# Optimization experiments

Hardware: AMD Instinct MI355X
Metric: run time of the kernel (lower is better)

## Reference

```python
import jax, jax.numpy as jnp
import numpy as np

B, N, C = 8, 2048, 256
H = 8
D = C // H
HID = 4 * C
EPS = 1e-5


def _layernorm(x, g, b):
    m = jnp.mean(x, axis=-1, keepdims=True)
    v = jnp.mean((x - m) ** 2, axis=-1, keepdims=True)
    return (x - m) * jax.lax.rsqrt(v + EPS) * g + b


def setup_inputs() -> dict:
    key = jax.random.key(0)
    ks = jax.random.split(key, 8)
    s = 0.02
    return {
        "x": jax.random.normal(ks[0], (B, N, C), dtype=jnp.float32),
        "ln1_g": jnp.ones((C,), jnp.float32),
        "ln1_b": jnp.zeros((C,), jnp.float32),
        "qkv_w": jax.random.normal(ks[1], (3 * C, C), jnp.float32) * s,  # torch Linear: (out,in), no bias
        "scale": jnp.asarray(D ** -0.5, jnp.float32),  # learnable temperature scalar
        "proj_w": jax.random.normal(ks[2], (C, C), jnp.float32) * s,
        "proj_b": jnp.zeros((C,), jnp.float32),
        "ln2_g": jnp.ones((C,), jnp.float32),
        "ln2_b": jnp.zeros((C,), jnp.float32),
        "fc1_w": jax.random.normal(ks[3], (HID, C), jnp.float32) * s,
        "fc1_b": jnp.zeros((HID,), jnp.float32),
        "fc2_w": jax.random.normal(ks[4], (C, HID), jnp.float32) * s,
        "fc2_b": jnp.zeros((C,), jnp.float32),
    }


def _attn(x, qkv_w, scale, proj_w, proj_b):
    b, n, c = x.shape
    qkv = (x @ qkv_w.T).reshape(b, n, 3, H, D)
    qkv = jnp.transpose(qkv, (2, 0, 3, 1, 4))  # (3, B, H, N, D)
    q, k, v = qkv[0], qkv[1], qkv[2]
    attn = jnp.einsum("bhnd,bhmd->bhnm", q, k) * scale  # full NxN scores (faithful)
    eye = jnp.eye(n, dtype=bool)
    attn = jnp.where(eye, -jnp.inf, attn)  # mask diagonal (no self-relation)
    attn = jax.nn.softmax(attn, axis=-1)
    out = jnp.einsum("bhnm,bhmd->bhnd", attn, v)
    out = jnp.transpose(out, (0, 2, 1, 3)).reshape(b, n, c)
    return out @ proj_w.T + proj_b


def reference(x, ln1_g, ln1_b, qkv_w, scale, proj_w, proj_b,
              ln2_g, ln2_b, fc1_w, fc1_b, fc2_w, fc2_b):
    x = x + _attn(_layernorm(x, ln1_g, ln1_b), qkv_w, scale, proj_w, proj_b)
    h = _layernorm(x, ln2_g, ln2_b)
    h = jax.nn.gelu(h @ fc1_w.T + fc1_b, approximate=False)  # torch GELU default = exact
    x = x + (h @ fc2_w.T + fc2_b)
    return x
```

## Files before the change

### kernel.cpp

```cpp
#include <hip/hip_runtime.h>
#include <cstdint>
#include <cstddef>


typedef __bf16 bf16x8 __attribute__((ext_vector_type(8)));
typedef __bf16 bf16x4 __attribute__((ext_vector_type(4)));
typedef float  f32x4  __attribute__((ext_vector_type(4)));

#define BN_TOK   2048
#define CC       256
#define HID_DIM  1024
#define MROWS    16384

#define OFF_W    0u
#define OFF_A    1572864u
#define OFF_QKV  9961472u
#define OFF_H    35127296u
#define WOFF_QKV 0
#define WOFF_PRJ 196608
#define WOFF_FC1 262144
#define WOFF_FC2 524288

__device__ __forceinline__ void gload_lds16(const __bf16* g, __bf16* l) {
    __builtin_amdgcn_global_load_lds(
        (const __attribute__((address_space(1))) void*)g,
        (__attribute__((address_space(3))) void*)l, 16, 0, 0);
}

__global__ __launch_bounds__(256) void cvt_w_kernel(
    const float* __restrict__ q, const float* __restrict__ p,
    const float* __restrict__ f1, const float* __restrict__ f2,
    __bf16* __restrict__ dst)
{
    int i = (blockIdx.x * 256 + threadIdx.x) * 4;
    const float* src; int off;
    if (i < 196608)      { src = q;  off = 0; }
    else if (i < 262144) { src = p;  off = 196608; }
    else if (i < 524288) { src = f1; off = 262144; }
    else                 { src = f2; off = 524288; }
    float4 v = *(const float4*)(src + (i - off));
    bf16x4 o;
    o[0] = (__bf16)v.x; o[1] = (__bf16)v.y; o[2] = (__bf16)v.z; o[3] = (__bf16)v.w;
    *(bf16x4*)(dst + i) = o;
}

__global__ __launch_bounds__(256) void ln_kernel(
    const float* __restrict__ x, const float* __restrict__ g,
    const float* __restrict__ b, __bf16* __restrict__ y)
{
    const int lane = threadIdx.x & 63;
    const int row  = blockIdx.x * 4 + (threadIdx.x >> 6);
    const float4 xv = *(const float4*)(x + (size_t)row * CC + lane * 4);
    float s  = xv.x + xv.y + xv.z + xv.w;
    float s2 = xv.x*xv.x + xv.y*xv.y + xv.z*xv.z + xv.w*xv.w;
#pragma unroll
    for (int m = 1; m < 64; m <<= 1) {
        s  += __shfl_xor(s,  m);
        s2 += __shfl_xor(s2, m);
    }
    const float mean = s * (1.0f / 256.0f);
    const float var  = fmaxf(s2 * (1.0f / 256.0f) - mean * mean, 0.0f);
    const float rstd = rsqrtf(var + 1e-5f);
    const float4 gv = *(const float4*)(g + lane * 4);
    const float4 bv = *(const float4*)(b + lane * 4);
    bf16x4 o;
    o[0] = (__bf16)((xv.x - mean) * rstd * gv.x + bv.x);
    o[1] = (__bf16)((xv.y - mean) * rstd * gv.y + bv.y);
    o[2] = (__bf16)((xv.z - mean) * rstd * gv.z + bv.z);
    o[3] = (__bf16)((xv.w - mean) * rstd * gv.w + bv.w);
    *(bf16x4*)(y + (size_t)row * CC + lane * 4) = o;
}

template<int BIAS, int GELU, int RES, int OUTBF>
__global__ __launch_bounds__(256) void gemm128(
    const __bf16* __restrict__ A, const __bf16* __restrict__ W,
    const float* __restrict__ bias, const float* __restrict__ res,
    void* __restrict__ outp, int M, int N, int K)
{
    __shared__ __align__(16) __bf16 As[128 * 32];
    __shared__ __align__(16) __bf16 Bs[128 * 32];
    const int tid = threadIdx.x, lane = tid & 63, wid = tid >> 6;
    const int wr = wid >> 1, wc = wid & 1;
    const int fr = lane & 15, fg = lane >> 4;
    const int tm = blockIdx.x * 128, tn = blockIdx.y * 128;

    const int lrow = lane >> 2, lk = (lane & 3) * 8;
    const __bf16* gA = A + (size_t)(tm + wid * 32 + lrow) * K + lk;
    const __bf16* gB = W + (size_t)(tn + wid * 32 + lrow) * K + lk;
    __bf16* lA = As + wid * 1024;
    __bf16* lB = Bs + wid * 1024;
    const size_t rowK16 = (size_t)16 * K;

    f32x4 acc[4][4];
    const f32x4 vz = {0.f, 0.f, 0.f, 0.f};
#pragma unroll
    for (int mi = 0; mi < 4; ++mi)
#pragma unroll
        for (int nj = 0; nj < 4; ++nj) acc[mi][nj] = vz;

    for (int k0 = 0; k0 < K; k0 += 32) {
        gload_lds16(gA + k0,          lA);
        gload_lds16(gA + rowK16 + k0, lA + 512);
        gload_lds16(gB + k0,          lB);
        gload_lds16(gB + rowK16 + k0, lB + 512);
        __syncthreads();
        bf16x8 af[4], bfv[4];
#pragma unroll
        for (int mi = 0; mi < 4; ++mi)
            af[mi] = *(const bf16x8*)&As[(wr * 64 + mi * 16 + fr) * 32 + fg * 8];
#pragma unroll
        for (int nj = 0; nj < 4; ++nj)
            bfv[nj] = *(const bf16x8*)&Bs[(wc * 64 + nj * 16 + fr) * 32 + fg * 8];
#pragma unroll
        for (int mi = 0; mi < 4; ++mi)
#pragma unroll
            for (int nj = 0; nj < 4; ++nj)
                acc[mi][nj] = __builtin_amdgcn_mfma_f32_16x16x32_bf16(
                    af[mi], bfv[nj], acc[mi][nj], 0, 0, 0);
        __syncthreads();
    }

#pragma unroll
    for (int mi = 0; mi < 4; ++mi) {
#pragma unroll
        for (int nj = 0; nj < 4; ++nj) {
            const int col = tn + wc * 64 + nj * 16 + fr;
            float bv = 0.0f;
            if (BIAS) bv = bias[col];
#pragma unroll
            for (int r = 0; r < 4; ++r) {
                const int row = tm + wr * 64 + mi * 16 + fg * 4 + r;
                float v = acc[mi][nj][r];
                if (BIAS) v += bv;
                if (GELU) v = v * 0.5f * (1.0f + erff(v * 0.70710678118654752f));
                if (RES)  v += res[(size_t)row * N + col];
                if (OUTBF) ((__bf16*)outp)[(size_t)row * N + col] = (__bf16)v;
                else       ((float*)outp)[(size_t)row * N + col]  = v;
            }
        }
    }
}

__global__ __launch_bounds__(256) void attn_kernel(
    const __bf16* __restrict__ qkv, const float* __restrict__ scale_p,
    __bf16* __restrict__ ao)
{
    __shared__ __align__(16) __bf16 Ks[64][40];
    __shared__ __align__(16) __bf16 Vt[32][72];
    __shared__ __align__(16) __bf16 Ps[4][32][72];

    const int tid = threadIdx.x, lane = tid & 63, wid = tid >> 6;
    const int fr = lane & 15, fg = lane >> 4;
    const int qt = blockIdx.x;
    const int bh = blockIdx.y;
    const int b = bh >> 3, h = bh & 7;
    const float c = scale_p[0] * 1.4426950408889634f;
    const size_t base = (size_t)b * BN_TOK * 768;
    const int hq = h * 32, hk = 256 + h * 32;
    const int ib = qt * 128 + wid * 32;

    bf16x8 qf[2];
    qf[0] = *(const bf16x8*)&qkv[base + (size_t)(ib + fr) * 768 + hq + fg * 8];
    qf[1] = *(const bf16x8*)&qkv[base + (size_t)(ib + 16 + fr) * 768 + hq + fg * 8];

    const f32x4 vz = {0.f, 0.f, 0.f, 0.f};
    f32x4 accd[2][2];
    accd[0][0] = vz; accd[0][1] = vz; accd[1][0] = vz; accd[1][1] = vz;
    float psum[2][4] = {{0.f,0.f,0.f,0.f},{0.f,0.f,0.f,0.f}};

    const int sj = tid >> 2, sd = (tid & 3) * 8;
    const __bf16* kptr = qkv + base + (size_t)sj * 768 + hk + sd;
    const __bf16* vptr = kptr + 256;

    for (int jt = 0; jt < 32; ++jt) {
        const int jb = jt * 64;
        __syncthreads();
        *(bf16x8*)&Ks[sj][sd] = *(const bf16x8*)kptr;
        const bf16x8 vv = *(const bf16x8*)vptr;
#pragma unroll
        for (int e = 0; e < 8; ++e) Vt[sd + e][sj] = vv[e];
        kptr += (size_t)64 * 768; vptr += (size_t)64 * 768;
        __syncthreads();

        const bool dmask = (jb < ib + 32) && (ib < jb + 64);

#pragma unroll
        for (int mi = 0; mi < 2; ++mi) {
            f32x4 s[4];
#pragma unroll
            for (int nj = 0; nj < 4; ++nj) {
                const bf16x8 kf = *(const bf16x8*)&Ks[nj * 16 + fr][fg * 8];
                s[nj] = __builtin_amdgcn_mfma_f32_16x16x32_bf16(qf[mi], kf, vz, 0, 0, 0);
            }
#pragma unroll
            for (int nj = 0; nj < 4; ++nj)
#pragma unroll
                for (int r = 0; r < 4; ++r)
                    s[nj][r] = exp2f(s[nj][r] * c);
            if (dmask) {
                const int gi = ib + mi * 16 + fg * 4;
#pragma unroll
                for (int nj = 0; nj < 4; ++nj) {
                    const int gj = jb + nj * 16 + fr;
#pragma unroll
                    for (int r = 0; r < 4; ++r)
                        if (gj == gi + r) s[nj][r] = 0.f;
                }
            }
#pragma unroll
            for (int nj = 0; nj < 4; ++nj)
#pragma unroll
                for (int r = 0; r < 4; ++r) {
                    psum[mi][r] += s[nj][r];
                    Ps[wid][mi * 16 + fg * 4 + r][nj * 16 + fr] = (__bf16)s[nj][r];
                }
        }
#pragma unroll
        for (int mi = 0; mi < 2; ++mi)
#pragma unroll
            for (int ka = 0; ka < 2; ++ka) {
                const bf16x8 pa = *(const bf16x8*)&Ps[wid][mi * 16 + fr][ka * 32 + fg * 8];
#pragma unroll
                for (int dh = 0; dh < 2; ++dh) {
                    const bf16x8 vb = *(const bf16x8*)&Vt[dh * 16 + fr][ka * 32 + fg * 8];
                    accd[mi][dh] = __builtin_amdgcn_mfma_f32_16x16x32_bf16(
                        pa, vb, accd[mi][dh], 0, 0, 0);
                }
            }
    }

#pragma unroll
    for (int mi = 0; mi < 2; ++mi)
#pragma unroll
        for (int r = 0; r < 4; ++r) {
            float s = psum[mi][r];
            s += __shfl_xor(s, 1); s += __shfl_xor(s, 2);
            s += __shfl_xor(s, 4); s += __shfl_xor(s, 8);
            psum[mi][r] = s;
        }
#pragma unroll
    for (int mi = 0; mi < 2; ++mi)
#pragma unroll
        for (int dh = 0; dh < 2; ++dh)
#pragma unroll
            for (int r = 0; r < 4; ++r) {
                const int i = ib + mi * 16 + fg * 4 + r;
                const float o = accd[mi][dh][r] / psum[mi][r];
                ao[(size_t)(b * BN_TOK + i) * CC + h * 32 + dh * 16 + fr] = (__bf16)o;
            }
}

extern "C" void kernel_launch(void* const* d_in, const int* in_sizes, int n_in,
                              void* d_out, int out_size, void* d_ws, size_t ws_size,
                              hipStream_t stream)
{
    const float* x      = (const float*)d_in[0];
    const float* ln1_g  = (const float*)d_in[1];
    const float* ln1_b  = (const float*)d_in[2];
    const float* qkv_w  = (const float*)d_in[3];
    const float* scale  = (const float*)d_in[4];
    const float* proj_w = (const float*)d_in[5];
    const float* proj_b = (const float*)d_in[6];
    const float* ln2_g  = (const float*)d_in[7];
    const float* ln2_b  = (const float*)d_in[8];
    const float* fc1_w  = (const float*)d_in[9];
    const float* fc1_b  = (const float*)d_in[10];
    const float* fc2_w  = (const float*)d_in[11];
    const float* fc2_b  = (const float*)d_in[12];

    char* ws = (char*)d_ws;
    __bf16* wbf   = (__bf16*)(ws + OFF_W);
    __bf16* abf   = (__bf16*)(ws + OFF_A);
    __bf16* qkvbf = (__bf16*)(ws + OFF_QKV);
    float*  x1    = (float*) (ws + OFF_QKV);
    __bf16* hbf   = (__bf16*)(ws + OFF_H);
    float*  out   = (float*)d_out;

    cvt_w_kernel<<<768, 256, 0, stream>>>(qkv_w, proj_w, fc1_w, fc2_w, wbf);
    ln_kernel<<<4096, 256, 0, stream>>>(x, ln1_g, ln1_b, abf);
    gemm128<0,0,0,1><<<dim3(128,6), 256, 0, stream>>>(
        abf, wbf + WOFF_QKV, nullptr, nullptr, qkvbf, MROWS, 768, 256);
    attn_kernel<<<dim3(16,64), 256, 0, stream>>>(qkvbf, scale, abf);
    gemm128<1,0,1,0><<<dim3(128,2), 256, 0, stream>>>(
        abf, wbf + WOFF_PRJ, proj_b, x, x1, MROWS, 256, 256);
    ln_kernel<<<4096, 256, 0, stream>>>(x1, ln2_g, ln2_b, abf);
    gemm128<1,1,0,1><<<dim3(128,8), 256, 0, stream>>>(
        abf, wbf + WOFF_FC1, fc1_b, nullptr, hbf, MROWS, HID_DIM, 256);
    gemm128<1,0,1,0><<<dim3(128,2), 256, 0, stream>>>(
        hbf, wbf + WOFF_FC2, fc2_b, x1, out, MROWS, 256, HID_DIM);
}
```

Baseline: 297.7 us.

## Transpose QK^T MFMA, swizzle P tile in LDS, hoist K/V fragment loads

The QK^T MFMA now runs with its operands swapped, so each lane holds four consecutive key scores for one query row. That lets P be written to LDS as packed 4-element bf16 vectors into an XOR-swizzled byte buffer, replacing scalar scattered stores. The row sum reduction shrinks to two shuffles plus a broadcast, the division becomes a multiply by a reciprocal, and the V transpose store order is permuted per thread to reduce LDS bank conflicts. K and V fragments are loaded once per tile and reused across both mi iterations, at the cost of more live registers.

```diff
diff --git a/kernel.cpp b/kernel.cpp
--- a/kernel.cpp
+++ b/kernel.cpp
@@ -147,7 +147,7 @@
 {
     __shared__ __align__(16) __bf16 Ks[64][40];
     __shared__ __align__(16) __bf16 Vt[32][72];
-    __shared__ __align__(16) __bf16 Ps[4][32][72];
+    __shared__ __align__(16) unsigned char PsT[4][32 * 128];
 
     const int tid = threadIdx.x, lane = tid & 63, wid = tid >> 6;
     const int fr = lane & 15, fg = lane >> 4;
@@ -166,11 +166,15 @@
     const f32x4 vz = {0.f, 0.f, 0.f, 0.f};
     f32x4 accd[2][2];
     accd[0][0] = vz; accd[0][1] = vz; accd[1][0] = vz; accd[1][1] = vz;
-    float psum[2][4] = {{0.f,0.f,0.f,0.f},{0.f,0.f,0.f,0.f}};
+    float psum[2] = {0.f, 0.f};
 
     const int sj = tid >> 2, sd = (tid & 3) * 8;
+    const int eperm = (tid & 3) << 1;
     const __bf16* kptr = qkv + base + (size_t)sj * 768 + hk + sd;
     const __bf16* vptr = kptr + 256;
+
+    unsigned char* pst = &PsT[wid][0];
+    const int swz = (fr & 7) << 4;
 
     for (int jt = 0; jt < 32; ++jt) {
         const int jb = jt * 64;
@@ -178,66 +182,84 @@
         *(bf16x8*)&Ks[sj][sd] = *(const bf16x8*)kptr;
         const bf16x8 vv = *(const bf16x8*)vptr;
 #pragma unroll
-        for (int e = 0; e < 8; ++e) Vt[sd + e][sj] = vv[e];
+        for (int t = 0; t < 8; ++t) {
+            const int e = t ^ eperm;
+            Vt[sd + e][sj] = vv[e];
+        }
         kptr += (size_t)64 * 768; vptr += (size_t)64 * 768;
         __syncthreads();
 
+        bf16x8 kf[4], vb[2][2];
+#pragma unroll
+        for (int nj = 0; nj < 4; ++nj)
+            kf[nj] = *(const bf16x8*)&Ks[nj * 16 + fr][fg * 8];
+#pragma unroll
+        for (int ka = 0; ka < 2; ++ka)
+#pragma unroll
+            for (int dh = 0; dh < 2; ++dh)
+                vb[ka][dh] = *(const bf16x8*)&Vt[dh * 16 + fr][ka * 32 + fg * 8];
+
         const bool dmask = (jb < ib + 32) && (ib < jb + 64);
 
 #pragma unroll
         for (int mi = 0; mi < 2; ++mi) {
             f32x4 s[4];
 #pragma unroll
-            for (int nj = 0; nj < 4; ++nj) {
-                const bf16x8 kf = *(const bf16x8*)&Ks[nj * 16 + fr][fg * 8];
-                s[nj] = __builtin_amdgcn_mfma_f32_16x16x32_bf16(qf[mi], kf, vz, 0, 0, 0);
-            }
+            for (int nj = 0; nj < 4; ++nj)
+                s[nj] = __builtin_amdgcn_mfma_f32_16x16x32_bf16(kf[nj], qf[mi], vz, 0, 0, 0);
 #pragma unroll
             for (int nj = 0; nj < 4; ++nj)
 #pragma unroll
                 for (int r = 0; r < 4; ++r)
                     s[nj][r] = exp2f(s[nj][r] * c);
             if (dmask) {
-                const int gi = ib + mi * 16 + fg * 4;
+                const int gi = ib + mi * 16 + fr;
 #pragma unroll
                 for (int nj = 0; nj < 4; ++nj) {
-                    const int gj = jb + nj * 16 + fr;
+                    const int gj = jb + nj * 16 + fg * 4;
 #pragma unroll
                     for (int r = 0; r < 4; ++r)
-                        if (gj == gi + r) s[nj][r] = 0.f;
+                        if (gj + r == gi) s[nj][r] = 0.f;
                 }
             }
-#pragma unroll
-            for (int nj = 0; nj < 4; ++nj)
-#pragma unroll
-                for (int r = 0; r < 4; ++r) {
-                    psum[mi][r] += s[nj][r];
-                    Ps[wid][mi * 16 + fg * 4 + r][nj * 16 + fr] = (__bf16)s[nj][r];
-                }
+            unsigned char* pr = pst + (mi * 16 + fr) * 128;
+#pragma unroll
+            for (int nj = 0; nj < 4; ++nj) {
+                psum[mi] += (s[nj][0] + s[nj][1]) + (s[nj][2] + s[nj][3]);
+                bf16x4 pk;
+                pk[0] = (__bf16)s[nj][0]; pk[1] = (__bf16)s[nj][1];
+                pk[2] = (__bf16)s[nj][2]; pk[3] = (__bf16)s[nj][3];
+                *(bf16x4*)(pr + ((nj * 32 + fg * 8) ^ swz)) = pk;
+            }
         }
 #pragma unroll
-        for (int mi = 0; mi < 2; ++mi)
+        for (int mi = 0; mi < 2; ++mi) {
+            unsigned char* pr = pst + (mi * 16 + fr) * 128;
 #pragma unroll
             for (int ka = 0; ka < 2; ++ka) {
-                const bf16x8 pa = *(const bf16x8*)&Ps[wid][mi * 16 + fr][ka * 32 + fg * 8];
-#pragma unroll
-                for (int dh = 0; dh < 2; ++dh) {
-                    const bf16x8 vb = *(const bf16x8*)&Vt[dh * 16 + fr][ka * 32 + fg * 8];
+                const bf16x8 pa = *(const bf16x8*)(pr + ((ka * 64 + fg * 16) ^ swz));
+#pragma unroll
+                for (int dh = 0; dh < 2; ++dh)
                     accd[mi][dh] = __builtin_amdgcn_mfma_f32_16x16x32_bf16(
-                        pa, vb, accd[mi][dh], 0, 0, 0);
-                }
-            }
-    }
-
+                        pa, vb[ka][dh], accd[mi][dh], 0, 0, 0);
+            }
+        }
+    }
+
+#pragma unroll
+    for (int mi = 0; mi < 2; ++mi) {
+        float p = psum[mi];
+        p += __shfl_xor(p, 16);
+        p += __shfl_xor(p, 32);
+        psum[mi] = p;
+    }
+    float rinv[2][4];
 #pragma unroll
     for (int mi = 0; mi < 2; ++mi)
 #pragma unroll
-        for (int r = 0; r < 4; ++r) {
-            float s = psum[mi][r];
-            s += __shfl_xor(s, 1); s += __shfl_xor(s, 2);
-            s += __shfl_xor(s, 4); s += __shfl_xor(s, 8);
-            psum[mi][r] = s;
-        }
+        for (int r = 0; r < 4; ++r)
+            rinv[mi][r] = 1.0f / __shfl(psum[mi], fg * 4 + r);
+
 #pragma unroll
     for (int mi = 0; mi < 2; ++mi)
 #pragma unroll
@@ -245,7 +267,7 @@
 #pragma unroll
             for (int r = 0; r < 4; ++r) {
                 const int i = ib + mi * 16 + fg * 4 + r;
-                const float o = accd[mi][dh][r] / psum[mi][r];
+                const float o = accd[mi][dh][r] * rinv[mi][r];
                 ao[(size_t)(b * BN_TOK + i) * CC + h * 32 + dh * 16 + fr] = (__bf16)o;
             }
 }
```

New measurement: 301.3 us. About the same (+1.2%).
